# Optimization experiments

Measured on AMD Instinct MI355X. Metric: run time of the kernel, lower is better.

The kernel has to match this reference:

```python
import jax, jax.numpy as jnp
import numpy as np

B, S, D, E, F = 4, 2048, 1024, 8, 4096


def setup_inputs() -> dict:
    key = jax.random.key(0)
    k1, k2, k3, k4 = jax.random.split(key, 4)
    x = jax.random.normal(k1, (B, S, D), dtype=jnp.float32)
    Wg = jax.random.normal(k2, (D, E), dtype=jnp.float32) / np.sqrt(D).astype(np.float32)
    w1 = jax.random.normal(k3, (E, D, F), dtype=jnp.float32) / np.sqrt(D).astype(np.float32)
    w2 = jax.random.normal(k4, (E, F, D), dtype=jnp.float32) / np.sqrt(F).astype(np.float32)
    return {"x": x, "Wg": Wg, "w1": w1, "w2": w2, "k": 2}


def reference(x, Wg, w1, w2, k):
    # x: [B, S, D] -> flatten tokens
    b, s, d = x.shape
    e = Wg.shape[1]
    xf = x.reshape(-1, d)                      # [T, D]
    t = xf.shape[0]
    logits = xf @ Wg                           # [T, E] gate logits
    topv, topi = jax.lax.top_k(logits, k)      # [T, k]
    # softmax over the top-k logits in float32, cast back (matches torch impl)
    w = jax.nn.softmax(topv.astype(jnp.float32), axis=-1).astype(x.dtype)
    # dense routing matrix [T, E]: weight for selected experts, 0 elsewhere
    route = jnp.zeros((t, e), dtype=x.dtype).at[jnp.arange(t)[:, None], topi].set(w)
    # per-expert FFN: y_e = gelu(x @ w1[e]) @ w2[e]; combine = sum_e route[:,e] * y_e
    out = jnp.zeros_like(xf)
    for ei in range(e):  # small fixed expert count
        h = jax.nn.gelu(xf @ w1[ei])           # [T, F]
        out = out + route[:, ei:ei + 1] * (h @ w2[ei])
    return out.reshape(b, s, d)
```

## Files before the change

kernel.cpp:

```cpp
#include <hip/hip_runtime.h>
#include <stdint.h>

#define T_TOK   8192
#define DMODEL  1024
#define NEXP    8
#define FFN     4096
#define TASSIGN 16384

typedef unsigned short u16;
typedef __attribute__((ext_vector_type(8))) short short8;
typedef __attribute__((ext_vector_type(8))) u16 u16x8;
typedef __attribute__((ext_vector_type(4))) u16 u16x4;
typedef __attribute__((ext_vector_type(4))) float f32x4;

__device__ __forceinline__ float bf2f(u16 u) {
  union { unsigned int i; float f; } v; v.i = ((unsigned int)u) << 16; return v.f;
}
__device__ __forceinline__ u16 f2bf(float f) {
  union { float f; unsigned int i; } v; v.f = f;
  unsigned int x = v.i;
  x += 0x7fffu + ((x >> 16) & 1u);
  return (u16)(x >> 16);
}
__device__ __forceinline__ float gelu_tanh(float x) {
  float z = 0.7978845608028654f * x * (1.0f + 0.044715f * x * x);
  float t = 1.0f - 2.0f / (__expf(2.0f * z) + 1.0f);
  return 0.5f * x * (1.0f + t);
}
__device__ __forceinline__ void async16(const void* g, void* l) {
  __builtin_amdgcn_global_load_lds((__attribute__((address_space(1))) void*)g,
                                   (__attribute__((address_space(3))) void*)l,
                                   16, 0, 0);
}

__global__ void init_kernel(int* __restrict__ meta) {
  if (threadIdx.x < 32) meta[threadIdx.x] = 0;
}

__global__ void gate_kernel(const float* __restrict__ x, const float* __restrict__ Wg,
                            int* __restrict__ topi, float* __restrict__ topw,
                            int* __restrict__ counts, u16* __restrict__ xb) {
  __shared__ float sWg[DMODEL * NEXP];
  int tid = threadIdx.x;
  for (int i = tid; i < DMODEL * NEXP / 4; i += 256)
    ((float4*)sWg)[i] = ((const float4*)Wg)[i];
  __syncthreads();

  int wave = tid >> 6, lane = tid & 63;
  int t = blockIdx.x * 4 + wave;

  float acc[NEXP] = {0, 0, 0, 0, 0, 0, 0, 0};
  const float* xr = x + (size_t)t * DMODEL;
  u16* xbr = xb + (size_t)t * DMODEL;
  for (int d0 = 0; d0 < DMODEL; d0 += 128) {
    int d = d0 + lane * 2;
    float2 xx = *(const float2*)(xr + d);
    *(uint32_t*)(xbr + d) = (uint32_t)f2bf(xx.x) | ((uint32_t)f2bf(xx.y) << 16);
    const float* g0 = sWg + (size_t)d * NEXP;
#pragma unroll
    for (int e = 0; e < NEXP; e++)
      acc[e] += xx.x * g0[e] + xx.y * g0[NEXP + e];
  }
#pragma unroll
  for (int off = 32; off > 0; off >>= 1)
#pragma unroll
    for (int e = 0; e < NEXP; e++)
      acc[e] += __shfl_xor(acc[e], off, 64);

  if (lane == 0) {
    float v0 = -1e30f, v1 = -1e30f; int i0 = 0, i1 = 0;
#pragma unroll
    for (int e = 0; e < NEXP; e++) {
      float v = acc[e];
      if (v > v0) { v1 = v0; i1 = i0; v0 = v; i0 = e; }
      else if (v > v1) { v1 = v; i1 = e; }
    }
    float e1 = __expf(v1 - v0);
    float s = 1.0f / (1.0f + e1);
    topi[t * 2] = i0; topi[t * 2 + 1] = i1;
    topw[t * 2] = s;  topw[t * 2 + 1] = e1 * s;
    atomicAdd(&counts[i0], 1);
    atomicAdd(&counts[i1], 1);
  }
}

__global__ void scan_kernel(const int* __restrict__ counts, int* __restrict__ offsets,
                            int* __restrict__ cursors) {
  if (threadIdx.x == 0) {
    int s = 0;
    for (int e = 0; e < NEXP; e++) { offsets[e] = s; s += counts[e]; }
    offsets[NEXP] = s;
  }
  if (threadIdx.x < NEXP) cursors[threadIdx.x] = 0;
}

__global__ void build_kernel(const int* __restrict__ topi, const int* __restrict__ offsets,
                             int* __restrict__ cursors, int* __restrict__ perm,
                             int* __restrict__ slotrow) {
  int t = blockIdx.x * blockDim.x + threadIdx.x;
  if (t >= T_TOK) return;
#pragma unroll
  for (int s = 0; s < 2; s++) {
    int e = topi[t * 2 + s];
    int p = atomicAdd(&cursors[e], 1);
    int g = offsets[e] + p;
    perm[g] = t;
    slotrow[t * 2 + s] = g;
  }
}

__global__ void transpose_kernel(const float* __restrict__ w1, const float* __restrict__ w2,
                                 u16* __restrict__ w1t, u16* __restrict__ w2t) {
  __shared__ u16 sh[64][72];
  int z = blockIdx.y;
  const float* src; u16* dst; int R, C;
  if (z < 8) { src = w1 + (size_t)z * (DMODEL * FFN); dst = w1t + (size_t)z * (FFN * DMODEL); R = DMODEL; C = FFN; }
  else       { src = w2 + (size_t)(z - 8) * (FFN * DMODEL); dst = w2t + (size_t)(z - 8) * (DMODEL * FFN); R = FFN; C = DMODEL; }
  int tilesC = C >> 6;
  int rt = blockIdx.x / tilesC, ct = blockIdx.x % tilesC;
  int tid = threadIdx.x;
#pragma unroll
  for (int i = 0; i < 2; i++) {
    int idx = i * 256 + tid;
    int r = idx >> 3, c8 = (idx & 7) * 8;
    const float* s = src + (size_t)(rt * 64 + r) * C + ct * 64 + c8;
    float4 v0 = *(const float4*)s, v1 = *(const float4*)(s + 4);
    u16* d = &sh[r][c8];
    d[0] = f2bf(v0.x); d[1] = f2bf(v0.y); d[2] = f2bf(v0.z); d[3] = f2bf(v0.w);
    d[4] = f2bf(v1.x); d[5] = f2bf(v1.y); d[6] = f2bf(v1.z); d[7] = f2bf(v1.w);
  }
  __syncthreads();
#pragma unroll
  for (int i = 0; i < 2; i++) {
    int idx = i * 256 + tid;
    int c = idx >> 3, r8 = (idx & 7) * 8;
    u16x8 v;
#pragma unroll
    for (int j = 0; j < 8; j++) v[j] = sh[r8 + j][c];
    *(u16x8*)(dst + (size_t)(ct * 64 + c) * R + rt * 64 + r8) = v;
  }
}

template <int K, int N, bool GATHER, bool GELU>
__global__ __launch_bounds__(512, 2) void gemm8_kernel(
    const u16* __restrict__ A, const u16* __restrict__ Bt, u16* __restrict__ C,
    const int* __restrict__ offsets, const int* __restrict__ perm) {
  __shared__ u16 S[65536];
  constexpr int NTT = N / 256;
  constexpr int MT  = 32;
  constexpr int NKT = K / 64;
  (void)NTT;

  int p = blockIdx.x;
  int e = p & 7;
  int slot = p >> 3;
  int ntile = slot / MT;
  int mtile = slot % MT;

  int off = offsets[e];
  int nrows = offsets[e + 1] - off;
  if (mtile * 256 >= nrows) return;

  int tid = threadIdx.x;
  int w = tid >> 6, l = tid & 63;
  int lm = l & 15, kq = l >> 4;
  int warp_m = w >> 2, warp_n = w & 3;
  int swz = (lm & 7) << 3;

  int scol8 = ((l & 7) ^ ((l >> 3) & 7)) * 8;
  int rbase = w * 8 + (l >> 3);
  const u16* aptr[2][2];
  const u16* bptr[2][2];
  const u16* bbase = Bt + (size_t)e * ((size_t)N * K);
#pragma unroll
  for (int q = 0; q < 2; q++)
#pragma unroll
    for (int i = 0; i < 2; i++) {
      int rr = rbase + i * 64;
      int rowA = (rr < 64 ? rr : rr + 64) + q * 64;
      int gm = mtile * 256 + rowA;
      int gmc = min(gm, nrows - 1);
      int arow = GATHER ? perm[off + gmc] : (off + gmc);
      aptr[q][i] = A + (size_t)arow * K + scol8;
      int rowB = ((rr >> 5) << 6) + (rr & 31) + q * 32;
      bptr[q][i] = bbase + (size_t)(ntile * 256 + rowB) * K + scol8;
    }
  int arb = w * 8;
  int brb = (w & 3) * 8 + (w >> 2) * 64;
  u16* As_lds = S;
  u16* Bs_lds = S + 32768;

#define STAGE_A(q, buf, kt) do {                                                       \
    async16(aptr[q][0] + (kt) * 64, As_lds + (buf) * 16384 + (arb + (q) * 64) * 64);   \
    async16(aptr[q][1] + (kt) * 64, As_lds + (buf) * 16384 + (arb + 128 + (q) * 64) * 64); \
  } while (0)
#define STAGE_B(q, buf, kt) do {                                                       \
    async16(bptr[q][0] + (kt) * 64, Bs_lds + (buf) * 16384 + (brb + (q) * 32) * 64);   \
    async16(bptr[q][1] + (kt) * 64, Bs_lds + (buf) * 16384 + (brb + 128 + (q) * 32) * 64); \
  } while (0)

  f32x4 acc[8][4];
  f32x4 zero = {0.f, 0.f, 0.f, 0.f};
#pragma unroll
  for (int i = 0; i < 8; i++)
#pragma unroll
    for (int j = 0; j < 4; j++) acc[i][j] = zero;

#define GEMM8_PHASE(BUF, QM, QN, STAGE_STMT, DO_VM)                                    \
  {                                                                                    \
    short8 af[4][2], bf[2][2];                                                         \
    const u16* ab = As_lds + (BUF) * 16384;                                            \
    const u16* bb = Bs_lds + (BUF) * 16384;                                            \
    _Pragma("unroll") for (int fi = 0; fi < 4; fi++) {                                 \
      int ml = warp_m * 128 + ((QM) * 4 + fi) * 16 + lm;                               \
      _Pragma("unroll") for (int ks = 0; ks < 2; ks++)                                 \
        af[fi][ks] = *(const short8*)(ab + ml * 64 + ((ks * 32 + kq * 8) ^ swz));      \
    }                                                                                  \
    _Pragma("unroll") for (int fj = 0; fj < 2; fj++) {                                 \
      int nl = warp_n * 64 + ((QN) * 2 + fj) * 16 + lm;                                \
      _Pragma("unroll") for (int ks = 0; ks < 2; ks++)                                 \
        bf[fj][ks] = *(const short8*)(bb + nl * 64 + ((ks * 32 + kq * 8) ^ swz));      \
    }                                                                                  \
    STAGE_STMT;                                                                        \
    __builtin_amdgcn_s_barrier();                                                      \
    asm volatile("s_waitcnt lgkmcnt(0)" ::: "memory");                                 \
    __builtin_amdgcn_sched_barrier(0);                                                 \
    __builtin_amdgcn_s_setprio(1);                                                     \
    _Pragma("unroll") for (int fi = 0; fi < 4; fi++)                                   \
      _Pragma("unroll") for (int fj = 0; fj < 2; fj++)                                 \
        _Pragma("unroll") for (int ks = 0; ks < 2; ks++)                               \
          acc[(QM) * 4 + fi][(QN) * 2 + fj] = __builtin_amdgcn_mfma_f32_16x16x32_bf16( \
              af[fi][ks], bf[fj][ks], acc[(QM) * 4 + fi][(QN) * 2 + fj], 0, 0, 0);     \
    __builtin_amdgcn_s_setprio(0);                                                     \
    if (DO_VM) asm volatile("s_waitcnt vmcnt(4)" ::: "memory");                        \
    __builtin_amdgcn_s_barrier();                                                      \
  }

  STAGE_A(0, 0, 0); STAGE_B(0, 0, 0); STAGE_A(1, 0, 0); STAGE_B(1, 0, 0);
  STAGE_A(0, 1, 1); STAGE_B(0, 1, 1);
  asm volatile("s_waitcnt vmcnt(4)" ::: "memory");
  __builtin_amdgcn_s_barrier();

  for (int it = 0; it < NKT / 2; it++) {
    int kt1 = 2 * it + 1;
    int t2 = min(2 * it + 2, NKT - 1);
    int t3 = min(2 * it + 3, NKT - 1);
    GEMM8_PHASE(0, 0, 0, STAGE_A(1, 1, kt1), 0)
    GEMM8_PHASE(0, 0, 1, STAGE_B(1, 1, kt1), 0)
    GEMM8_PHASE(0, 1, 0, STAGE_A(0, 0, t2), 0)
    GEMM8_PHASE(0, 1, 1, STAGE_B(0, 0, t2), 1)
    GEMM8_PHASE(1, 0, 0, STAGE_A(1, 0, t2), 0)
    GEMM8_PHASE(1, 0, 1, STAGE_B(1, 0, t2), 0)
    GEMM8_PHASE(1, 1, 0, STAGE_A(0, 1, t3), 0)
    GEMM8_PHASE(1, 1, 1, STAGE_B(0, 1, t3), 1)
  }

  asm volatile("s_waitcnt vmcnt(0)" ::: "memory");

#pragma unroll
  for (int fi = 0; fi < 8; fi++) {
    int rowb = mtile * 256 + warp_m * 128 + fi * 16 + kq * 4;
#pragma unroll
    for (int r = 0; r < 4; r++) {
      int row = rowb + r;
      if (row < nrows) {
        u16* crow = C + (size_t)(off + row) * N + ntile * 256 + warp_n * 64 + lm;
#pragma unroll
        for (int fj = 0; fj < 4; fj++) {
          float v = acc[fi][fj][r];
          if (GELU) v = gelu_tanh(v);
          crow[fj * 16] = f2bf(v);
        }
      }
    }
  }
#undef STAGE_A
#undef STAGE_B
#undef GEMM8_PHASE
}

template <int K, int N, bool GATHER, bool GELU>
__global__ __launch_bounds__(256) void gemm_f_kernel(
    const u16* __restrict__ A, const float* __restrict__ B, u16* __restrict__ C,
    const int* __restrict__ offsets, const int* __restrict__ perm) {
  __shared__ u16 As[128 * 32];
  __shared__ u16 Bs[128 * 32];
  int e = blockIdx.z;
  int off = offsets[e];
  int nrows = offsets[e + 1] - off;
  int mtile = blockIdx.y;
  if (mtile * 128 >= nrows) return;
  int ntile = blockIdx.x;

  int tid = threadIdx.x;
  int wave = tid >> 6, lane = tid & 63;

  int rr = tid >> 2;
  int kc = (tid & 3) * 8;
  int m0 = mtile * 128 + rr;
  int mm0 = min(m0, nrows - 1);
  int mm1 = min(m0 + 64, nrows - 1);
  const u16 *arow0, *arow1;
  if (GATHER) {
    arow0 = A + (size_t)perm[off + mm0] * K + kc;
    arow1 = A + (size_t)perm[off + mm1] * K + kc;
  } else {
    arow0 = A + (size_t)(off + mm0) * K + kc;
    arow1 = A + (size_t)(off + mm1) * K + kc;
  }

  int kk2 = (tid >> 4) * 2;
  int n8  = (tid & 15) * 8;
  const float* brow0 = B + (size_t)e * ((size_t)K * N) + (size_t)kk2 * N
                         + (size_t)ntile * 128 + n8;
  const float* brow1 = brow0 + N;

  int wm = (wave >> 1) * 64, wn = (wave & 1) * 64;
  int lm = lane & 15, kq = lane >> 4;

  f32x4 acc[4][4];
  f32x4 zero = {0.f, 0.f, 0.f, 0.f};
#pragma unroll
  for (int i = 0; i < 4; i++)
#pragma unroll
    for (int j = 0; j < 4; j++) acc[i][j] = zero;

  uint32_t* bs32 = (uint32_t*)Bs;
  for (int k0 = 0; k0 < K; k0 += 32) {
    u16x8 av0 = *(const u16x8*)(arow0 + k0);
    u16x8 av1 = *(const u16x8*)(arow1 + k0);
    float4 b00 = *(const float4*)(brow0 + (size_t)k0 * N);
    float4 b01 = *(const float4*)(brow0 + (size_t)k0 * N + 4);
    float4 b10 = *(const float4*)(brow1 + (size_t)k0 * N);
    float4 b11 = *(const float4*)(brow1 + (size_t)k0 * N + 4);
    __syncthreads();
    *(u16x8*)(As + (size_t)rr * 32 + kc) = av0;
    *(u16x8*)(As + (size_t)(rr + 64) * 32 + kc) = av1;
    int wcol = kk2 >> 1;
    bs32[(size_t)(n8 + 0) * 16 + wcol] = (uint32_t)f2bf(b00.x) | ((uint32_t)f2bf(b10.x) << 16);
    bs32[(size_t)(n8 + 1) * 16 + wcol] = (uint32_t)f2bf(b00.y) | ((uint32_t)f2bf(b10.y) << 16);
    bs32[(size_t)(n8 + 2) * 16 + wcol] = (uint32_t)f2bf(b00.z) | ((uint32_t)f2bf(b10.z) << 16);
    bs32[(size_t)(n8 + 3) * 16 + wcol] = (uint32_t)f2bf(b00.w) | ((uint32_t)f2bf(b10.w) << 16);
    bs32[(size_t)(n8 + 4) * 16 + wcol] = (uint32_t)f2bf(b01.x) | ((uint32_t)f2bf(b11.x) << 16);
    bs32[(size_t)(n8 + 5) * 16 + wcol] = (uint32_t)f2bf(b01.y) | ((uint32_t)f2bf(b11.y) << 16);
    bs32[(size_t)(n8 + 6) * 16 + wcol] = (uint32_t)f2bf(b01.z) | ((uint32_t)f2bf(b11.z) << 16);
    bs32[(size_t)(n8 + 7) * 16 + wcol] = (uint32_t)f2bf(b01.w) | ((uint32_t)f2bf(b11.w) << 16);
    __syncthreads();
    short8 a[4], b[4];
#pragma unroll
    for (int i = 0; i < 4; i++) {
      a[i] = *(const short8*)(As + (size_t)(wm + i * 16 + lm) * 32 + kq * 8);
      b[i] = *(const short8*)(Bs + (size_t)(wn + i * 16 + lm) * 32 + kq * 8);
    }
#pragma unroll
    for (int i = 0; i < 4; i++)
#pragma unroll
      for (int j = 0; j < 4; j++)
        acc[i][j] = __builtin_amdgcn_mfma_f32_16x16x32_bf16(a[i], b[j], acc[i][j], 0, 0, 0);
  }

#pragma unroll
  for (int i = 0; i < 4; i++) {
    int rbase = mtile * 128 + wm + i * 16 + kq * 4;
#pragma unroll
    for (int r = 0; r < 4; r++) {
      int row = rbase + r;
      if (row < nrows) {
        u16* crow = C + (size_t)(off + row) * N + ntile * 128 + wn + lm;
#pragma unroll
        for (int j = 0; j < 4; j++) {
          float v = acc[i][j][r];
          if (GELU) v = gelu_tanh(v);
          crow[j * 16] = f2bf(v);
        }
      }
    }
  }
}

__global__ void combine_kernel(const u16* __restrict__ Y, const int* __restrict__ slotrow,
                               const float* __restrict__ topw, float* __restrict__ out) {
  int idx = blockIdx.x * 256 + threadIdx.x;
  int t = idx >> 8;
  int c = (idx & 255) * 4;
  int g0 = slotrow[t * 2], g1 = slotrow[t * 2 + 1];
  float w0 = topw[t * 2], w1 = topw[t * 2 + 1];
  u16x4 y0 = *(const u16x4*)(Y + (size_t)g0 * DMODEL + c);
  u16x4 y1 = *(const u16x4*)(Y + (size_t)g1 * DMODEL + c);
  float4 o;
  o.x = w0 * bf2f(y0[0]) + w1 * bf2f(y1[0]);
  o.y = w0 * bf2f(y0[1]) + w1 * bf2f(y1[1]);
  o.z = w0 * bf2f(y0[2]) + w1 * bf2f(y1[2]);
  o.w = w0 * bf2f(y0[3]) + w1 * bf2f(y1[3]);
  *(float4*)(out + (size_t)t * DMODEL + c) = o;
}

extern "C" void kernel_launch(void* const* d_in, const int* in_sizes, int n_in,
                              void* d_out, int out_size, void* d_ws, size_t ws_size,
                              hipStream_t stream) {
  const float* x  = (const float*)d_in[0];
  const float* Wg = (const float*)d_in[1];
  const float* w1 = (const float*)d_in[2];
  const float* w2 = (const float*)d_in[3];
  float* out = (float*)d_out;

  const size_t SZ_H   = (size_t)TASSIGN * FFN * 2;
  const size_t SZ_W1T = (size_t)NEXP * FFN * DMODEL * 2;
  const size_t SZ_W2T = (size_t)NEXP * DMODEL * FFN * 2;
  const size_t SZ_XB  = (size_t)T_TOK * DMODEL * 2;
  const size_t SZ_Y   = (size_t)TASSIGN * DMODEL * 2;
  const size_t SZ_SMALL = (size_t)TASSIGN * 4 * 4 + 4096;
  const size_t WS_FULL = SZ_H + SZ_W1T + SZ_W2T + SZ_XB + SZ_SMALL;

  uint8_t* ws = (uint8_t*)d_ws;
  bool fast = (ws_size >= WS_FULL);

  size_t o = 0;
  u16* H = (u16*)(ws + o); o += SZ_H;
  u16 *w1t = nullptr, *w2t = nullptr, *Y;
  if (fast) {
    w1t = (u16*)(ws + o); o += SZ_W1T;
    w2t = (u16*)(ws + o); o += SZ_W2T;
    Y = w1t;
  } else {
    Y = (u16*)(ws + o); o += SZ_Y;
  }
  u16* xb = (u16*)(ws + o); o += SZ_XB;
  int*   topi    = (int*)(ws + o);   o += (size_t)TASSIGN * 4;
  float* topw    = (float*)(ws + o); o += (size_t)TASSIGN * 4;
  int*   perm    = (int*)(ws + o);   o += (size_t)TASSIGN * 4;
  int*   slotrow = (int*)(ws + o);   o += (size_t)TASSIGN * 4;
  int*   meta    = (int*)(ws + o);
  int* counts = meta, *offsets = meta + 8, *cursors = meta + 17;

  init_kernel<<<1, 64, 0, stream>>>(meta);
  gate_kernel<<<T_TOK / 4, 256, 0, stream>>>(x, Wg, topi, topw, counts, xb);
  scan_kernel<<<1, 64, 0, stream>>>(counts, offsets, cursors);
  build_kernel<<<T_TOK / 256, 256, 0, stream>>>(topi, offsets, cursors, perm, slotrow);

  if (fast) {
    transpose_kernel<<<dim3(1024, 16), 256, 0, stream>>>(w1, w2, w1t, w2t);
    gemm8_kernel<DMODEL, FFN, true, true>
        <<<NEXP * (FFN / 256) * 32, 512, 0, stream>>>(xb, w1t, H, offsets, perm);
    gemm8_kernel<FFN, DMODEL, false, false>
        <<<NEXP * (DMODEL / 256) * 32, 512, 0, stream>>>(H, w2t, Y, offsets, perm);
  } else {
    gemm_f_kernel<DMODEL, FFN, true, true>
        <<<dim3(FFN / 128, 64, NEXP), 256, 0, stream>>>(xb, w1, H, offsets, perm);
    gemm_f_kernel<FFN, DMODEL, false, false>
        <<<dim3(DMODEL / 128, 64, NEXP), 256, 0, stream>>>(H, w2, Y, offsets, perm);
  }
  combine_kernel<<<(T_TOK * DMODEL / 4) / 256, 256, 0, stream>>>(Y, slotrow, topw, out);
}
```

Baseline: 1.064 ms.

## Reorder quadrant traversal to reuse LDS fragments and restage the prefetch pipeline

Restructures the 256x256 bf16 MFMA GEMM main loop. Quadrants are now visited in a serpentine order (00,01,11,10) so A or B fragments read from LDS carry over between consecutive phases, roughly halving LDS fragment reads. The async global-to-LDS stage issues are reassigned across phases, with a different prologue and vmcnt wait depth. The aim is to cut LDS read traffic and the per-phase barrier overhead, at the cost of more live registers and a more fragile buffer hazard schedule.

```diff
diff --git a/kernel.cpp b/kernel.cpp
--- a/kernel.cpp
+++ b/kernel.cpp
@@ -206,53 +206,57 @@
 #pragma unroll
     for (int j = 0; j < 4; j++) acc[i][j] = zero;
 
-#define GEMM8_PHASE(BUF, QM, QN, STAGE_STMT, DO_VM)                                    \
-  {                                                                                    \
-    short8 af[4][2], bf[2][2];                                                         \
-    const u16* ab = As_lds + (BUF) * 16384;                                            \
-    const u16* bb = Bs_lds + (BUF) * 16384;                                            \
-    _Pragma("unroll") for (int fi = 0; fi < 4; fi++) {                                 \
-      int ml = warp_m * 128 + ((QM) * 4 + fi) * 16 + lm;                               \
+  short8 af[4][2], b0[2][2], b1[2][2];
+
+#define RD_A(BUF, QM)                                                                  \
+  _Pragma("unroll") for (int fi = 0; fi < 4; fi++) {                                   \
+    int ml = warp_m * 128 + ((QM) * 4 + fi) * 16 + lm;                                 \
+    _Pragma("unroll") for (int ks = 0; ks < 2; ks++)                                   \
+      af[fi][ks] = *(const short8*)(As_lds + (BUF) * 16384 + ml * 64 +                 \
+                                    ((ks * 32 + kq * 8) ^ swz));                       \
+  }
+#define RD_B(BUF, QN, BV)                                                              \
+  _Pragma("unroll") for (int fj = 0; fj < 2; fj++) {                                   \
+    int nl = warp_n * 64 + ((QN) * 2 + fj) * 16 + lm;                                  \
+    _Pragma("unroll") for (int ks = 0; ks < 2; ks++)                                   \
+      BV[fj][ks] = *(const short8*)(Bs_lds + (BUF) * 16384 + nl * 64 +                 \
+                                    ((ks * 32 + kq * 8) ^ swz));                       \
+  }
+#define MM(QM, QN, BV)                                                                 \
+  __builtin_amdgcn_s_barrier();                                                        \
+  asm volatile("s_waitcnt lgkmcnt(0)" ::: "memory");                                   \
+  __builtin_amdgcn_sched_barrier(0);                                                   \
+  __builtin_amdgcn_s_setprio(1);                                                       \
+  _Pragma("unroll") for (int fi = 0; fi < 4; fi++)                                     \
+    _Pragma("unroll") for (int fj = 0; fj < 2; fj++)                                   \
       _Pragma("unroll") for (int ks = 0; ks < 2; ks++)                                 \
-        af[fi][ks] = *(const short8*)(ab + ml * 64 + ((ks * 32 + kq * 8) ^ swz));      \
-    }                                                                                  \
-    _Pragma("unroll") for (int fj = 0; fj < 2; fj++) {                                 \
-      int nl = warp_n * 64 + ((QN) * 2 + fj) * 16 + lm;                                \
-      _Pragma("unroll") for (int ks = 0; ks < 2; ks++)                                 \
-        bf[fj][ks] = *(const short8*)(bb + nl * 64 + ((ks * 32 + kq * 8) ^ swz));      \
-    }                                                                                  \
-    STAGE_STMT;                                                                        \
-    __builtin_amdgcn_s_barrier();                                                      \
-    asm volatile("s_waitcnt lgkmcnt(0)" ::: "memory");                                 \
-    __builtin_amdgcn_sched_barrier(0);                                                 \
-    __builtin_amdgcn_s_setprio(1);                                                     \
-    _Pragma("unroll") for (int fi = 0; fi < 4; fi++)                                   \
-      _Pragma("unroll") for (int fj = 0; fj < 2; fj++)                                 \
-        _Pragma("unroll") for (int ks = 0; ks < 2; ks++)                               \
-          acc[(QM) * 4 + fi][(QN) * 2 + fj] = __builtin_amdgcn_mfma_f32_16x16x32_bf16( \
-              af[fi][ks], bf[fj][ks], acc[(QM) * 4 + fi][(QN) * 2 + fj], 0, 0, 0);     \
-    __builtin_amdgcn_s_setprio(0);                                                     \
-    if (DO_VM) asm volatile("s_waitcnt vmcnt(4)" ::: "memory");                        \
-    __builtin_amdgcn_s_barrier();                                                      \
-  }
-
-  STAGE_A(0, 0, 0); STAGE_B(0, 0, 0); STAGE_A(1, 0, 0); STAGE_B(1, 0, 0);
-  STAGE_A(0, 1, 1); STAGE_B(0, 1, 1);
-  asm volatile("s_waitcnt vmcnt(4)" ::: "memory");
+        acc[(QM) * 4 + fi][(QN) * 2 + fj] = __builtin_amdgcn_mfma_f32_16x16x32_bf16(   \
+            af[fi][ks], BV[fj][ks], acc[(QM) * 4 + fi][(QN) * 2 + fj], 0, 0, 0);       \
+  __builtin_amdgcn_s_setprio(0);
+
+#define TILE(BUF, OBUF, KT1, KT2)                                                      \
+  RD_A(BUF, 0) RD_B(BUF, 0, b0) STAGE_B(0, OBUF, KT1);                                 \
+  MM(0, 0, b0) __builtin_amdgcn_s_barrier();                                           \
+  RD_B(BUF, 1, b1) STAGE_A(0, BUF, KT2);                                               \
+  MM(0, 1, b1) __builtin_amdgcn_s_barrier();                                           \
+  RD_A(BUF, 1) STAGE_B(1, BUF, KT2);                                                   \
+  MM(1, 1, b1) __builtin_amdgcn_s_barrier();                                           \
+  RD_B(BUF, 0, b0) STAGE_A(1, BUF, KT2);                                               \
+  MM(1, 0, b0)                                                                         \
+  asm volatile("s_waitcnt vmcnt(4)" ::: "memory");                                     \
+  __builtin_amdgcn_s_barrier();
+
+  STAGE_A(0, 0, 0); STAGE_B(0, 0, 0); STAGE_B(1, 0, 0); STAGE_A(1, 0, 0);
+  STAGE_A(0, 1, 1); STAGE_B(1, 1, 1); STAGE_A(1, 1, 1);
+  asm volatile("s_waitcnt vmcnt(6)" ::: "memory");
   __builtin_amdgcn_s_barrier();
 
   for (int it = 0; it < NKT / 2; it++) {
     int kt1 = 2 * it + 1;
     int t2 = min(2 * it + 2, NKT - 1);
     int t3 = min(2 * it + 3, NKT - 1);
-    GEMM8_PHASE(0, 0, 0, STAGE_A(1, 1, kt1), 0)
-    GEMM8_PHASE(0, 0, 1, STAGE_B(1, 1, kt1), 0)
-    GEMM8_PHASE(0, 1, 0, STAGE_A(0, 0, t2), 0)
-    GEMM8_PHASE(0, 1, 1, STAGE_B(0, 0, t2), 1)
-    GEMM8_PHASE(1, 0, 0, STAGE_A(1, 0, t2), 0)
-    GEMM8_PHASE(1, 0, 1, STAGE_B(1, 0, t2), 0)
-    GEMM8_PHASE(1, 1, 0, STAGE_A(0, 1, t3), 0)
-    GEMM8_PHASE(1, 1, 1, STAGE_B(0, 1, t3), 1)
+    TILE(0, 1, kt1, t2)
+    TILE(1, 0, t2, t3)
   }
 
   asm volatile("s_waitcnt vmcnt(0)" ::: "memory");
@@ -276,7 +280,10 @@
   }
 #undef STAGE_A
 #undef STAGE_B
-#undef GEMM8_PHASE
+#undef RD_A
+#undef RD_B
+#undef MM
+#undef TILE
 }
 
 template <int K, int N, bool GATHER, bool GELU>
```

Result: faster. 1.018 ms (-4.3%).
